# Kernel tuning notes

Measured on AMD Instinct MI355X. Metric: run time of the kernel, lower is better.

Reference implementation:

```python
import jax, jax.numpy as jnp
from jax import lax
import numpy as np

B, N, C = 64, 8732, 81  # batch, anchors (SSD300), classes (COCO+bg)
POS_RATE = 0.003        # keep 3*num_pos < N (argsort column index must be in range)


def setup_inputs() -> dict:
    key = jax.random.key(0)
    k1, k2, k3, k4, k5, k6 = jax.random.split(key, 6)
    pred_conf = jax.random.normal(k1, (B, N, C), dtype=jnp.float32)
    pred_loc = jax.random.normal(k2, (B, N, 4), dtype=jnp.float32)
    # one-hot gt_conf; class 0 = background; sparse positives
    is_pos = jax.random.uniform(k3, (B, N)) < POS_RATE
    labels = jnp.where(is_pos, jax.random.randint(k4, (B, N), 1, C), 0)
    gt_conf = jax.nn.one_hot(labels, C, dtype=jnp.float32)
    gt_loc = jax.random.normal(k5, (B, N, 4), dtype=jnp.float32)
    return {"pred_conf": pred_conf, "pred_loc": pred_loc,
            "gt_conf": gt_conf, "gt_loc": gt_loc}


def reference(pred_conf, pred_loc, gt_conf, gt_loc):
    negative_ratio = 3.0
    # softmax cross entropy per anchor: [B, N]
    log_sm = jax.nn.log_softmax(pred_conf, axis=-1)
    conf_loss = -jnp.sum(log_sm * gt_conf, axis=-1)

    # positive mask (gt background prob == 0 => positive); detached in original
    pos_mask = (lax.stop_gradient(gt_conf)[:, :, 0] == 0).astype(jnp.float32)
    num_pos = jnp.sum(pos_mask)
    positive_conf_loss = pos_mask * conf_loss

    # hard-negative mining (faithful to original, including the quirk that the
    # "threshold" is the argsort INDEX value at column num_negative_conf)
    neg_mask = 1.0 - pos_mask
    cl_neg = lax.stop_gradient(conf_loss) * neg_mask  # detached in original
    order = jnp.argsort(cl_neg, axis=-1)              # [B, N] ascending
    num_neg = (negative_ratio * num_pos).astype(jnp.int32)  # scalar, traced
    idx = jnp.broadcast_to(num_neg, (cl_neg.shape[0], 1))
    thr = jnp.take_along_axis(order, idx, axis=1).astype(jnp.float32)  # [B,1]
    neg_mask = neg_mask * (cl_neg > thr).astype(jnp.float32)
    negative_conf_loss = neg_mask * conf_loss

    conf_total = jnp.sum(positive_conf_loss + negative_conf_loss, axis=-1)  # [B]

    # smooth-L1-ish loc loss (faithful, incl. loc_loss_mask == linear mask bug)
    d = pred_loc - gt_loc
    lin = (jnp.abs(lax.stop_gradient(d)) > 1.0).astype(jnp.float32)
    loc = ((jnp.abs(d) - 0.5) * lin + 0.5 * d * d * (1.0 - lin)) * lin
    loc_total = jnp.sum(loc, axis=(-1, -2))  # [B]

    return conf_total, loc_total
```

## Files before the change

kernel.cpp:

```cpp
#include <hip/hip_runtime.h>
#include <hip/hip_bf16.h>
#include <math.h>

#define NCLS 81
#define NANCH 8732
#define NB 64
#define BUCKET_STRIDE 16
#define TILE_F 5184
#define TILE_F4 1296
#define HSTRIDE 257

__global__ __launch_bounds__(256) void conf_kernel(
    const float* __restrict__ pred_conf,
    const float* __restrict__ gt_conf,
    float* __restrict__ cl_out,
    int* __restrict__ pos_buckets,
    float* __restrict__ row_pos)
{
    __shared__ float sx[TILE_F];
    __shared__ int label_s[64];
    __shared__ int pcnt[4];

    const int tid = threadIdx.x;
    const int lane = tid & 63, wid = tid >> 6;
    const size_t tbase = (size_t)blockIdx.x * TILE_F;
    const float4* p4 = (const float4*)(pred_conf + tbase);
    const float4* g4 = (const float4*)(gt_conf + tbase);

    for (int c = wid; c < 21; c += 4) {
        int f4 = c * 64 + lane;
        if (f4 < TILE_F4) {
            __builtin_amdgcn_global_load_lds(
                (const __attribute__((address_space(1))) unsigned int*)(p4 + f4),
                (__attribute__((address_space(3))) unsigned int*)(&sx[f4 * 4]),
                16, 0, 0);
        }
    }

    int mycnt = 0;
#pragma unroll
    for (int i = 0; i < 6; ++i) {
        int k = tid + 256 * i;
        if (k < TILE_F4) {
            float4 g = g4[k];
            int base = 4 * k;
            float gv[4] = {g.x, g.y, g.z, g.w};
#pragma unroll
            for (int t = 0; t < 4; ++t) {
                if (gv[t] != 0.0f) {
                    int gidx = base + t;
                    int a = gidx / NCLS;
                    int cls = gidx - a * NCLS;
                    label_s[a] = cls;
                    mycnt += (cls != 0);
                }
            }
        }
    }
    for (int off = 32; off; off >>= 1) mycnt += __shfl_xor(mycnt, off);
    if (lane == 0) pcnt[wid] = mycnt;

    __syncthreads();

    const int a = tid >> 2;
    const int q = tid & 3;
    const float* xr = sx + a * NCLS;

    float s0 = 0.f, s1 = 0.f, s2 = 0.f;
#pragma unroll
    for (int j = 0; j < 21; ++j) {
        int c = q + 4 * j;
        if (c < NCLS) {
            float e = __expf(xr[c]);
            if (j % 3 == 0) s0 += e; else if (j % 3 == 1) s1 += e; else s2 += e;
        }
    }
    float s = s0 + s1 + s2;
    s += __shfl_xor(s, 1);
    s += __shfl_xor(s, 2);
    const float lse = __logf(s);

    const int anchor = blockIdx.x * 64 + a;
    float conf_loss = 0.f;
    bool posf = false;
    if (q == 0) {
        int lbl = label_s[a];
        conf_loss = lse - xr[lbl];
        posf = (lbl != 0);
        cl_out[anchor] = posf ? 0.0f : conf_loss;
    }

    const int b = anchor / NANCH;
    const float contrib = posf ? conf_loss : 0.0f;
    const int bF = __builtin_amdgcn_readfirstlane(b);
    float c0 = (b == bF) ? contrib : 0.0f;
    float c1 = contrib - c0;
    for (int off = 32; off; off >>= 1) {
        c0 += __shfl_xor(c0, off);
        c1 += __shfl_xor(c1, off);
    }
    if (lane == 0) {
        if (c0 != 0.f) atomicAdd(&row_pos[bF], c0);
        if (c1 != 0.f) atomicAdd(&row_pos[bF + 1], c1);
    }
    if (tid == 0) {
        int tot = pcnt[0] + pcnt[1] + pcnt[2] + pcnt[3];
        if (tot) atomicAdd(&pos_buckets[(blockIdx.x & 63) * BUCKET_STRIDE], tot);
    }
}

__global__ __launch_bounds__(256) void loc_kernel(
    const float* __restrict__ pred_loc,
    const float* __restrict__ gt_loc,
    float* __restrict__ out)
{
    __shared__ float red[4];
    const int b = blockIdx.y;
    const int idx = blockIdx.x * 256 + threadIdx.x;
    float local = 0.f;
    if (idx < NANCH) {
        const float4* p = (const float4*)(pred_loc + (long long)b * (NANCH * 4));
        const float4* g = (const float4*)(gt_loc + (long long)b * (NANCH * 4));
        float4 pv = p[idx];
        float4 gv = g[idx];
        float a0 = fabsf(pv.x - gv.x), a1 = fabsf(pv.y - gv.y);
        float a2 = fabsf(pv.z - gv.z), a3 = fabsf(pv.w - gv.w);
        local  = (a0 > 1.f) ? (a0 - 0.5f) : 0.f;
        local += (a1 > 1.f) ? (a1 - 0.5f) : 0.f;
        local += (a2 > 1.f) ? (a2 - 0.5f) : 0.f;
        local += (a3 > 1.f) ? (a3 - 0.5f) : 0.f;
    }
    for (int off = 32; off; off >>= 1) local += __shfl_xor(local, off);
    if ((threadIdx.x & 63) == 0) red[threadIdx.x >> 6] = local;
    __syncthreads();
    if (threadIdx.x == 0)
        atomicAdd(&out[64 + b], red[0] + red[1] + red[2] + red[3]);
}

__global__ __launch_bounds__(1024) void select_kernel(
    const float* __restrict__ val,
    const int* __restrict__ pos_buckets,
    const float* __restrict__ row_pos,
    float* __restrict__ out)
{
    __shared__ float cl[NANCH];
    __shared__ int hist[4 * HSTRIDE];
    __shared__ int wsum[16];
    __shared__ float fred[16];
    __shared__ int sh_numpos;
    __shared__ unsigned int sh_prefix;
    __shared__ int sh_k, sh_thr;

    const int b = blockIdx.x;
    const int tid = threadIdx.x;
    const int lane = tid & 63, w = tid >> 6;
    const int hofs = (w & 3) * HSTRIDE;
    const float* row = val + b * NANCH;

    if (tid < 64) {
        int v = pos_buckets[tid * BUCKET_STRIDE];
        for (int off = 32; off; off >>= 1) v += __shfl_xor(v, off);
        if (tid == 0) sh_numpos = v;
    }
    for (int i = tid; i < NANCH; i += 1024) cl[i] = row[i];
    __syncthreads();

    int k = 3 * sh_numpos;
    if (k > NANCH - 1) k = NANCH - 1;
    if (k < 0) k = 0;

    unsigned int prefix = 0u;
    for (int r = 0; r < 4; ++r) {
        const int shift = 24 - 8 * r;
        const unsigned int maskHigh = (r == 0) ? 0u : (0xFFFFFFFFu << (shift + 8));
        for (int j = tid; j < 4 * HSTRIDE; j += 1024) hist[j] = 0;
        __syncthreads();
        if (r == 0) {
            for (int i0 = 0; i0 < 9216; i0 += 1024) {
                int i = i0 + tid;
                bool valid = (i < NANCH);
                unsigned int u = valid ? __float_as_uint(cl[i]) : 0u;
                int bin = (int)(u >> 24);
                unsigned long long act = __ballot(valid);
                while (act) {
                    int leader = (int)__ffsll((long long)act) - 1;
                    int lbin = __shfl(bin, leader);
                    unsigned long long sm = __ballot(valid && (bin == lbin));
                    if (lane == leader) atomicAdd(&hist[hofs + lbin], (int)__popcll(sm));
                    act &= ~sm;
                }
            }
        } else {
            for (int i = tid; i < NANCH; i += 1024) {
                unsigned int u = __float_as_uint(cl[i]);
                if ((u & maskHigh) == prefix)
                    atomicAdd(&hist[hofs + ((u >> shift) & 0xFF)], 1);
            }
        }
        __syncthreads();
        int h = 0, v = 0;
        if (tid < 256) {
            h = hist[tid] + hist[HSTRIDE + tid] + hist[2 * HSTRIDE + tid]
              + hist[3 * HSTRIDE + tid];
            v = h;
#pragma unroll
            for (int off = 1; off < 64; off <<= 1) {
                int u2 = __shfl_up(v, off);
                if (lane >= off) v += u2;
            }
            if (lane == 63) wsum[w] = v;
        }
        __syncthreads();
        if (tid < 256) {
            int add = 0;
            for (int i = 0; i < w; ++i) add += wsum[i];
            int incl = v + add, excl = incl - h;
            if (excl <= k && k < incl) {
                sh_prefix = prefix | ((unsigned int)tid << shift);
                sh_k = k - excl;
            }
        }
        __syncthreads();
        prefix = sh_prefix;
        k = sh_k;
        __syncthreads();
    }
    const unsigned int T = prefix;

    const int CHUNK = 9;
    int lo = tid * CHUNK; if (lo > NANCH) lo = NANCH;
    int hi = lo + CHUNK; if (hi > NANCH) hi = NANCH;
    int cnt = 0;
    for (int i = lo; i < hi; ++i)
        cnt += (__float_as_uint(cl[i]) == T);
    int v2 = cnt;
#pragma unroll
    for (int off = 1; off < 64; off <<= 1) {
        int u2 = __shfl_up(v2, off);
        if (lane >= off) v2 += u2;
    }
    if (lane == 63) wsum[w] = v2;
    __syncthreads();
    if (tid < 16) {
        int s = wsum[tid];
#pragma unroll
        for (int off = 1; off < 16; off <<= 1) {
            int u2 = __shfl_up(s, off);
            if (lane >= off) s += u2;
        }
        wsum[tid] = s;
    }
    __syncthreads();
    {
        int add = (w == 0) ? 0 : wsum[w - 1];
        int incl = v2 + add, excl = incl - cnt;
        if (excl <= k && k < incl) {
            int need = k - excl, idx = NANCH - 1;
            for (int i = lo; i < hi; ++i) {
                if (__float_as_uint(cl[i]) == T) {
                    if (need == 0) { idx = i; break; }
                    --need;
                }
            }
            sh_thr = idx;
        }
    }
    __syncthreads();

    const float thr = (float)sh_thr;
    float local = 0.f;
    for (int i = tid; i < NANCH; i += 1024) {
        float c = cl[i];
        if (c > thr) local += c;
    }
    for (int off = 32; off; off >>= 1) local += __shfl_xor(local, off);
    if (lane == 0) fred[w] = local;
    __syncthreads();
    if (tid == 0) {
        float t = row_pos[b];
        for (int i = 0; i < 16; ++i) t += fred[i];
        out[b] = t;
    }
}

extern "C" void kernel_launch(void* const* d_in, const int* in_sizes, int n_in,
                              void* d_out, int out_size, void* d_ws, size_t ws_size,
                              hipStream_t stream) {
    const float* pred_conf = (const float*)d_in[0];
    const float* pred_loc  = (const float*)d_in[1];
    const float* gt_conf   = (const float*)d_in[2];
    const float* gt_loc    = (const float*)d_in[3];
    float* out = (float*)d_out;

    int*   pos_buckets = (int*)d_ws;
    float* row_pos     = (float*)((char*)d_ws + 4096);
    float* vals        = (float*)((char*)d_ws + 8192);

    hipMemsetAsync(d_ws, 0, 8192, stream);
    hipMemsetAsync(d_out, 0, 128 * sizeof(float), stream);

    conf_kernel<<<NANCH, 256, 0, stream>>>(pred_conf, gt_conf, vals,
                                           pos_buckets, row_pos);
    loc_kernel<<<dim3((NANCH + 255) / 256, NB), 256, 0, stream>>>(pred_loc, gt_loc, out);
    select_kernel<<<NB, 1024, 0, stream>>>(vals, pos_buckets, row_pos, out);
}
```

Baseline: 403.0 us.

## Fuse loc loss into conf kernel and read conf rows directly without LDS staging

Merges the loc-loss reduction into the conf kernel as extra blocks, which removes one kernel launch and lets both kinds of block run at the same time. The conf path no longer stages pred_conf in LDS with async loads and no longer scans gt_conf for the label. Each quad of threads now reads its anchor's row straight from global memory with misaligned-head float4 loads, and computes the cross-entropy as lse minus the dot product with the one-hot vector. Positive counting moves to per-wave atomics, which means more atomics and less coalesced global access in exchange for no LDS and no block barriers.

Result: slower. 429.8 us (+6.7%).

```diff
diff --git a/kernel.cpp b/kernel.cpp
--- a/kernel.cpp
+++ b/kernel.cpp
@@ -1,140 +1,109 @@
 #include <hip/hip_runtime.h>
-#include <hip/hip_bf16.h>
 #include <math.h>
 
 #define NCLS 81
 #define NANCH 8732
 #define NB 64
 #define BUCKET_STRIDE 16
-#define TILE_F 5184
-#define TILE_F4 1296
 #define HSTRIDE 257
-
-__global__ __launch_bounds__(256) void conf_kernel(
+#define NCONF_BLK 8732
+#define NLOC_BLK  2240
+
+__global__ __launch_bounds__(256) void conf_loc_kernel(
     const float* __restrict__ pred_conf,
     const float* __restrict__ gt_conf,
+    const float* __restrict__ pred_loc,
+    const float* __restrict__ gt_loc,
     float* __restrict__ cl_out,
     int* __restrict__ pos_buckets,
-    float* __restrict__ row_pos)
+    float* __restrict__ row_pos,
+    float* __restrict__ out)
 {
-    __shared__ float sx[TILE_F];
-    __shared__ int label_s[64];
-    __shared__ int pcnt[4];
-
     const int tid = threadIdx.x;
     const int lane = tid & 63, wid = tid >> 6;
-    const size_t tbase = (size_t)blockIdx.x * TILE_F;
-    const float4* p4 = (const float4*)(pred_conf + tbase);
-    const float4* g4 = (const float4*)(gt_conf + tbase);
-
-    for (int c = wid; c < 21; c += 4) {
-        int f4 = c * 64 + lane;
-        if (f4 < TILE_F4) {
-            __builtin_amdgcn_global_load_lds(
-                (const __attribute__((address_space(1))) unsigned int*)(p4 + f4),
-                (__attribute__((address_space(3))) unsigned int*)(&sx[f4 * 4]),
-                16, 0, 0);
-        }
-    }
-
-    int mycnt = 0;
-#pragma unroll
-    for (int i = 0; i < 6; ++i) {
-        int k = tid + 256 * i;
-        if (k < TILE_F4) {
+
+    if (blockIdx.x >= NCONF_BLK) {
+        const int bid = blockIdx.x - NCONF_BLK;
+        const int b = bid & 63;
+        const int chunk = bid >> 6;
+        const int idx = chunk * 256 + tid;
+        float local = 0.f;
+        if (idx < NANCH) {
+            const float4* p = (const float4*)(pred_loc + (size_t)b * (NANCH * 4));
+            const float4* g = (const float4*)(gt_loc + (size_t)b * (NANCH * 4));
+            float4 pv = p[idx];
+            float4 gv = g[idx];
+            float a0 = fabsf(pv.x - gv.x), a1 = fabsf(pv.y - gv.y);
+            float a2 = fabsf(pv.z - gv.z), a3 = fabsf(pv.w - gv.w);
+            local  = (a0 > 1.f) ? (a0 - 0.5f) : 0.f;
+            local += (a1 > 1.f) ? (a1 - 0.5f) : 0.f;
+            local += (a2 > 1.f) ? (a2 - 0.5f) : 0.f;
+            local += (a3 > 1.f) ? (a3 - 0.5f) : 0.f;
+        }
+        for (int off = 32; off; off >>= 1) local += __shfl_xor(local, off);
+        if (lane == 0 && local != 0.f) atomicAdd(&out[64 + b], local);
+        return;
+    }
+
+    const int a_loc = tid >> 2;
+    const int q = tid & 3;
+    const int anchor = blockIdx.x * 64 + a_loc;
+    const int h = (4 - (anchor & 3)) & 3;
+    const size_t fbase = (size_t)anchor * NCLS;
+    const float* xr = pred_conf + fbase;
+    const float* gr = gt_conf + fbase;
+    const float4* x4 = (const float4*)(xr + h);
+    const float4* g4 = (const float4*)(gr + h);
+    const int n4 = (NCLS - h) >> 2;
+
+    float se = 0.f, dot = 0.f, g0v = 1.0f;
+#pragma unroll
+    for (int j = 0; j < 5; ++j) {
+        const int k = 4 * j + q;
+        if (k < n4) {
+            float4 x = x4[k];
             float4 g = g4[k];
-            int base = 4 * k;
-            float gv[4] = {g.x, g.y, g.z, g.w};
-#pragma unroll
-            for (int t = 0; t < 4; ++t) {
-                if (gv[t] != 0.0f) {
-                    int gidx = base + t;
-                    int a = gidx / NCLS;
-                    int cls = gidx - a * NCLS;
-                    label_s[a] = cls;
-                    mycnt += (cls != 0);
-                }
-            }
-        }
-    }
-    for (int off = 32; off; off >>= 1) mycnt += __shfl_xor(mycnt, off);
-    if (lane == 0) pcnt[wid] = mycnt;
-
-    __syncthreads();
-
-    const int a = tid >> 2;
-    const int q = tid & 3;
-    const float* xr = sx + a * NCLS;
-
-    float s0 = 0.f, s1 = 0.f, s2 = 0.f;
-#pragma unroll
-    for (int j = 0; j < 21; ++j) {
-        int c = q + 4 * j;
-        if (c < NCLS) {
-            float e = __expf(xr[c]);
-            if (j % 3 == 0) s0 += e; else if (j % 3 == 1) s1 += e; else s2 += e;
-        }
-    }
-    float s = s0 + s1 + s2;
-    s += __shfl_xor(s, 1);
-    s += __shfl_xor(s, 2);
-    const float lse = __logf(s);
-
-    const int anchor = blockIdx.x * 64 + a;
-    float conf_loss = 0.f;
+            se  += __expf(x.x) + __expf(x.y) + __expf(x.z) + __expf(x.w);
+            dot += x.x * g.x + x.y * g.y + x.z * g.z + x.w * g.w;
+            if (j == 0 && q == 0 && h == 0) g0v = g.x;
+        }
+    }
+    const int cnt = NCLS - 4 * n4;
+    for (int i = q; i < cnt; i += 4) {
+        const int e = (i < h) ? i : (h + 4 * n4 + (i - h));
+        float xv = xr[e], gv = gr[e];
+        se  += __expf(xv);
+        dot += xv * gv;
+        if (e == 0) g0v = gv;
+    }
+
+    se  += __shfl_xor(se, 1);  dot += __shfl_xor(dot, 1);
+    se  += __shfl_xor(se, 2);  dot += __shfl_xor(dot, 2);
+    const float lse = __logf(se);
+    const float conf_loss = lse - dot;
+
     bool posf = false;
     if (q == 0) {
-        int lbl = label_s[a];
-        conf_loss = lse - xr[lbl];
-        posf = (lbl != 0);
+        posf = (g0v == 0.0f);
         cl_out[anchor] = posf ? 0.0f : conf_loss;
     }
 
     const int b = anchor / NANCH;
-    const float contrib = posf ? conf_loss : 0.0f;
+    float contrib = (q == 0 && posf) ? conf_loss : 0.0f;
+    int pc = (q == 0 && posf) ? 1 : 0;
     const int bF = __builtin_amdgcn_readfirstlane(b);
     float c0 = (b == bF) ? contrib : 0.0f;
     float c1 = contrib - c0;
     for (int off = 32; off; off >>= 1) {
         c0 += __shfl_xor(c0, off);
         c1 += __shfl_xor(c1, off);
+        pc += __shfl_xor(pc, off);
     }
     if (lane == 0) {
         if (c0 != 0.f) atomicAdd(&row_pos[bF], c0);
         if (c1 != 0.f) atomicAdd(&row_pos[bF + 1], c1);
-    }
-    if (tid == 0) {
-        int tot = pcnt[0] + pcnt[1] + pcnt[2] + pcnt[3];
-        if (tot) atomicAdd(&pos_buckets[(blockIdx.x & 63) * BUCKET_STRIDE], tot);
-    }
-}
-
-__global__ __launch_bounds__(256) void loc_kernel(
-    const float* __restrict__ pred_loc,
-    const float* __restrict__ gt_loc,
-    float* __restrict__ out)
-{
-    __shared__ float red[4];
-    const int b = blockIdx.y;
-    const int idx = blockIdx.x * 256 + threadIdx.x;
-    float local = 0.f;
-    if (idx < NANCH) {
-        const float4* p = (const float4*)(pred_loc + (long long)b * (NANCH * 4));
-        const float4* g = (const float4*)(gt_loc + (long long)b * (NANCH * 4));
-        float4 pv = p[idx];
-        float4 gv = g[idx];
-        float a0 = fabsf(pv.x - gv.x), a1 = fabsf(pv.y - gv.y);
-        float a2 = fabsf(pv.z - gv.z), a3 = fabsf(pv.w - gv.w);
-        local  = (a0 > 1.f) ? (a0 - 0.5f) : 0.f;
-        local += (a1 > 1.f) ? (a1 - 0.5f) : 0.f;
-        local += (a2 > 1.f) ? (a2 - 0.5f) : 0.f;
-        local += (a3 > 1.f) ? (a3 - 0.5f) : 0.f;
-    }
-    for (int off = 32; off; off >>= 1) local += __shfl_xor(local, off);
-    if ((threadIdx.x & 63) == 0) red[threadIdx.x >> 6] = local;
-    __syncthreads();
-    if (threadIdx.x == 0)
-        atomicAdd(&out[64 + b], red[0] + red[1] + red[2] + red[3]);
+        if (pc) atomicAdd(&pos_buckets[(((blockIdx.x << 2) | wid) & 63) * BUCKET_STRIDE], pc);
+    }
 }
 
 __global__ __launch_bounds__(1024) void select_kernel(
@@ -299,8 +268,7 @@
     hipMemsetAsync(d_ws, 0, 8192, stream);
     hipMemsetAsync(d_out, 0, 128 * sizeof(float), stream);
 
-    conf_kernel<<<NANCH, 256, 0, stream>>>(pred_conf, gt_conf, vals,
-                                           pos_buckets, row_pos);
-    loc_kernel<<<dim3((NANCH + 255) / 256, NB), 256, 0, stream>>>(pred_loc, gt_loc, out);
+    conf_loc_kernel<<<NCONF_BLK + NLOC_BLK, 256, 0, stream>>>(
+        pred_conf, gt_conf, pred_loc, gt_loc, vals, pos_buckets, row_pos, out);
     select_kernel<<<NB, 1024, 0, stream>>>(vals, pos_buckets, row_pos, out);
 }
```
